# Optimization experiments

Hardware: AMD Instinct MI355X
Metric: run time of the kernel (lower is better)

Reference implementation:

```python
import jax, jax.numpy as jnp
import numpy as np

N_NODES = 50000
N_EDGES = 800000
HEADS = 4
OUT_CH = 64
NEG_SLOPE = 0.2  # PyG GATConv default


def gat_conv(x, edge_index, W, att_src, att_dst, bias):
    """PyG GATConv (concat=True, add_self_loops=True, eval mode).
    x: [N, F_in], edge_index: [2, E] (row 0 = src, row 1 = dst).
    W: [F_in, H*C], att_src/att_dst: [1, H, C], bias: [H*C].
    """
    n = x.shape[0]
    loops = jnp.arange(n, dtype=edge_index.dtype)
    src = jnp.concatenate([edge_index[0], loops])  # [E+N]
    dst = jnp.concatenate([edge_index[1], loops])

    h = (x @ W).reshape(n, HEADS, OUT_CH)           # [N, H, C]
    a_src = jnp.sum(h * att_src, axis=-1)           # [N, H]
    a_dst = jnp.sum(h * att_dst, axis=-1)           # [N, H]

    e = a_src[src] + a_dst[dst]                     # [E+N, H]
    e = jax.nn.leaky_relu(e, NEG_SLOPE)

    # segment softmax over incoming edges of each dst node
    e_max = jax.ops.segment_max(e, dst, num_segments=n)   # [N, H]
    e_exp = jnp.exp(e - e_max[dst])
    denom = jax.ops.segment_sum(e_exp, dst, num_segments=n)
    alpha = e_exp / (denom[dst] + 1e-16)            # [E+N, H]

    msg = h[src] * alpha[:, :, None]                # [E+N, H, C]
    out = jax.ops.segment_sum(msg, dst, num_segments=n)   # [N, H, C]
    return out.reshape(n, HEADS * OUT_CH) + bias


def setup_inputs() -> dict:
    key = jax.random.key(0)
    ks = jax.random.split(key, 10)
    d_in = 256
    d_hid = HEADS * OUT_CH  # 256
    s_in = 1.0 / np.sqrt(d_in)
    s_hid = 1.0 / np.sqrt(d_hid)
    return {
        "x": jax.random.normal(ks[0], (N_NODES, d_in), dtype=jnp.float32),
        "edge_index": jax.random.randint(ks[1], (2, N_EDGES), 0, N_NODES, dtype=jnp.int32),
        "W1": jax.random.normal(ks[2], (d_in, d_hid), dtype=jnp.float32) * s_in,
        "att_src1": jax.random.normal(ks[3], (1, HEADS, OUT_CH), dtype=jnp.float32) * s_hid,
        "att_dst1": jax.random.normal(ks[4], (1, HEADS, OUT_CH), dtype=jnp.float32) * s_hid,
        "b1": jnp.zeros((d_hid,), dtype=jnp.float32),
        "W2": jax.random.normal(ks[5], (d_hid, d_hid), dtype=jnp.float32) * s_hid,
        "att_src2": jax.random.normal(ks[6], (1, HEADS, OUT_CH), dtype=jnp.float32) * s_hid,
        "att_dst2": jax.random.normal(ks[7], (1, HEADS, OUT_CH), dtype=jnp.float32) * s_hid,
        "b2": jnp.zeros((d_hid,), dtype=jnp.float32),
    }


def reference(x, edge_index, W1, att_src1, att_dst1, b1, W2, att_src2, att_dst2, b2):
    # layer 1 + ELU (dropout is identity in eval mode)
    h = gat_conv(x, edge_index, W1, att_src1, att_dst1, b1)
    h = jax.nn.elu(h)
    # layer 2 + ELU
    h = gat_conv(h, edge_index, W2, att_src2, att_dst2, b2)
    h = jax.nn.elu(h)
    return h
```

## Files before the change

### kernel.cpp

```cpp
#include <hip/hip_runtime.h>
#include <hip/hip_bf16.h>

#define N_NODES 50000
#define N_EDGES 800000

typedef __attribute__((ext_vector_type(8))) short short8;
typedef __attribute__((ext_vector_type(4))) float floatx4;

__device__ __forceinline__ ushort f2bf(float f) {
    uint u = __float_as_uint(f);
    uint r = u + 0x7FFFu + ((u >> 16) & 1u);
    return (ushort)(r >> 16);
}
__device__ __forceinline__ float bfu2f(ushort h) {
    return __uint_as_float(((uint)h) << 16);
}
__device__ __forceinline__ float bflo(uint u) { return __uint_as_float(u << 16); }
__device__ __forceinline__ float bfhi(uint u) { return __uint_as_float(u & 0xffff0000u); }
__device__ __forceinline__ float lrelu(float e) { return e >= 0.f ? e : 0.2f * e; }

__global__ void deg_kernel(const int* __restrict__ dst, int* __restrict__ cnt, int E) {
    int i = blockIdx.x * blockDim.x + threadIdx.x;
    if (i < E) atomicAdd(&cnt[dst[i]], 1);
}

__global__ __launch_bounds__(256) void scan1_kernel(const int* __restrict__ cnt,
                                                    int* __restrict__ excl,
                                                    int* __restrict__ partial, int n) {
    __shared__ int sd[256];
    int tid = threadIdx.x;
    int i = blockIdx.x * 256 + tid;
    int v = (i < n) ? cnt[i] : 0;
    sd[tid] = v;
    __syncthreads();
    #pragma unroll
    for (int off = 1; off < 256; off <<= 1) {
        int t = (tid >= off) ? sd[tid - off] : 0;
        __syncthreads();
        sd[tid] += t;
        __syncthreads();
    }
    if (i < n) excl[i] = sd[tid] - v;
    if (tid == 255) partial[blockIdx.x] = sd[255];
}

__global__ __launch_bounds__(256) void scan2_kernel(int* __restrict__ partial, int nb) {
    __shared__ int sd[256];
    int tid = threadIdx.x;
    int v = (tid < nb) ? partial[tid] : 0;
    sd[tid] = v;
    __syncthreads();
    #pragma unroll
    for (int off = 1; off < 256; off <<= 1) {
        int t = (tid >= off) ? sd[tid - off] : 0;
        __syncthreads();
        sd[tid] += t;
        __syncthreads();
    }
    if (tid < nb) partial[tid] = sd[tid] - v;
}

__global__ __launch_bounds__(256) void scan3_kernel(const int* __restrict__ excl,
                                                    const int* __restrict__ partial,
                                                    int* __restrict__ row_ptr,
                                                    int* __restrict__ row_tmp, int n) {
    int i = blockIdx.x * 256 + threadIdx.x;
    if (i < n) {
        int v = excl[i] + partial[blockIdx.x];
        row_ptr[i] = v;
        row_tmp[i] = v;
    }
    if (i == 0) row_ptr[n] = N_EDGES;
}

__global__ void scatter_kernel(const int* __restrict__ src, const int* __restrict__ dst,
                               int* __restrict__ row_tmp, int* __restrict__ sorted_src,
                               int* __restrict__ sorted_dst, int E) {
    int i = blockIdx.x * blockDim.x + threadIdx.x;
    if (i < E) {
        int d = dst[i];
        int p = atomicAdd(&row_tmp[d], 1);
        sorted_src[p] = src[i];
        sorted_dst[p] = d;
    }
}

__global__ void prep_w(const float* __restrict__ W1, const float* __restrict__ W2,
                       ushort* __restrict__ Wt1_hi, ushort* __restrict__ Wt1_lo,
                       ushort* __restrict__ Wt2_hi, ushort* __restrict__ Wt2_lo) {
    int n = threadIdx.x, k = blockIdx.x & 255;
    const float* W = (blockIdx.x < 256) ? W1 : W2;
    ushort* Wh = (blockIdx.x < 256) ? Wt1_hi : Wt2_hi;
    ushort* Wl = (blockIdx.x < 256) ? Wt1_lo : Wt2_lo;
    float v = W[k * 256 + n];
    ushort hb = f2bf(v);
    Wh[n * 256 + k] = hb;
    Wl[n * 256 + k] = f2bf(v - bfu2f(hb));
}

__global__ __launch_bounds__(256) void gemm_att_kernel(const float* __restrict__ A,
                                                       const ushort* __restrict__ Wt_hi,
                                                       const ushort* __restrict__ Wt_lo,
                                                       const float* __restrict__ att_s,
                                                       const float* __restrict__ att_d,
                                                       ushort* __restrict__ H,
                                                       float* __restrict__ a_src,
                                                       float* __restrict__ a_dst, int M) {
    const int ROWP = 40;
    __shared__ ushort hi_s[128 * ROWP];
    __shared__ ushort lo_s[128 * ROWP];
    const int tid = threadIdx.x;
    const int wave = tid >> 6, lane = tid & 63;
    const int quad = lane >> 4, l16 = lane & 15;
    const int brow = blockIdx.x * 64;
    const int coff = blockIdx.y * 128;
    const int mrow = brow + wave * 16 + l16;
    const int mload = (mrow < M) ? mrow : (M - 1);

    floatx4 acc[8];
    #pragma unroll
    for (int t = 0; t < 8; t++) acc[t] = (floatx4){0.f, 0.f, 0.f, 0.f};

    for (int k0 = 0; k0 < 256; k0 += 32) {
        __syncthreads();
        {
            int t = tid & 127;
            const ushort* g = ((tid < 128) ? Wt_hi : Wt_lo) + (size_t)(coff + t) * 256 + k0;
            ushort* d = ((tid < 128) ? hi_s : lo_s) + t * ROWP;
            #pragma unroll
            for (int i = 0; i < 4; i++)
                *reinterpret_cast<short8*>(d + i * 8) =
                    *reinterpret_cast<const short8*>(g + i * 8);
        }
        __syncthreads();
        const float* ap = A + (size_t)mload * 256 + k0 + quad * 8;
        float4 a0 = *reinterpret_cast<const float4*>(ap);
        float4 a1 = *reinterpret_cast<const float4*>(ap + 4);
        float av[8] = {a0.x, a0.y, a0.z, a0.w, a1.x, a1.y, a1.z, a1.w};
        short8 a_hi, a_lo;
        #pragma unroll
        for (int j = 0; j < 8; j++) {
            ushort hb = f2bf(av[j]);
            a_hi[j] = (short)hb;
            a_lo[j] = (short)f2bf(av[j] - bfu2f(hb));
        }
        #pragma unroll
        for (int t = 0; t < 8; t++) {
            int roff = (t * 16 + l16) * ROWP + quad * 8;
            short8 b_hi = *reinterpret_cast<const short8*>(&hi_s[roff]);
            short8 b_lo = *reinterpret_cast<const short8*>(&lo_s[roff]);
            acc[t] = __builtin_amdgcn_mfma_f32_16x16x32_bf16(a_hi, b_hi, acc[t], 0, 0, 0);
            acc[t] = __builtin_amdgcn_mfma_f32_16x16x32_bf16(a_hi, b_lo, acc[t], 0, 0, 0);
            acc[t] = __builtin_amdgcn_mfma_f32_16x16x32_bf16(a_lo, b_hi, acc[t], 0, 0, 0);
        }
    }
    const int hb = blockIdx.y * 2;
    float ps[2][4] = {}, pd[2][4] = {};
    #pragma unroll
    for (int t = 0; t < 8; t++) {
        int hh = t >> 2;
        float as_v = att_s[coff + t * 16 + l16];
        float ad_v = att_d[coff + t * 16 + l16];
        #pragma unroll
        for (int r = 0; r < 4; r++) {
            ps[hh][r] += acc[t][r] * as_v;
            pd[hh][r] += acc[t][r] * ad_v;
        }
    }
    #pragma unroll
    for (int off = 1; off < 16; off <<= 1) {
        #pragma unroll
        for (int hh = 0; hh < 2; hh++)
            #pragma unroll
            for (int r = 0; r < 4; r++) {
                ps[hh][r] += __shfl_xor(ps[hh][r], off, 64);
                pd[hh][r] += __shfl_xor(pd[hh][r], off, 64);
            }
    }
    if (l16 == 0) {
        #pragma unroll
        for (int r = 0; r < 4; r++) {
            int m = brow + wave * 16 + quad * 4 + r;
            if (m < M) {
                #pragma unroll
                for (int hh = 0; hh < 2; hh++) {
                    a_src[m * 4 + hb + hh] = ps[hh][r];
                    a_dst[m * 4 + hb + hh] = pd[hh][r];
                }
            }
        }
    }
    #pragma unroll
    for (int t = 0; t < 8; t++) {
        int col = coff + t * 16 + l16;
        int c = col & 63, hh = col >> 6;
        #pragma unroll
        for (int r = 0; r < 4; r++) {
            int m = brow + wave * 16 + quad * 4 + r;
            if (m < M) H[(size_t)m * 256 + c * 4 + hh] = f2bf(acc[t][r]);
        }
    }
}

__global__ __launch_bounds__(256) void ew_kernel(const float* __restrict__ a_src,
                                                 const float* __restrict__ a_dst,
                                                 const int* __restrict__ sorted_src,
                                                 const int* __restrict__ sorted_dst,
                                                 float* __restrict__ ew, int E) {
    int j = blockIdx.x * 256 + threadIdx.x;
    if (j >= E) return;
    int s = sorted_src[j], d = sorted_dst[j];
    float4 as_ = *reinterpret_cast<const float4*>(a_src + (size_t)s * 4);
    float4 ad_ = *reinterpret_cast<const float4*>(a_dst + (size_t)d * 4);
    float4 w;
    w.x = __expf(lrelu(as_.x + ad_.x));
    w.y = __expf(lrelu(as_.y + ad_.y));
    w.z = __expf(lrelu(as_.z + ad_.z));
    w.w = __expf(lrelu(as_.w + ad_.w));
    *reinterpret_cast<float4*>(ew + (size_t)j * 4) = w;
}

__global__ __launch_bounds__(256) void agg_kernel(const ushort* __restrict__ H,
                                                  const float* __restrict__ a_src,
                                                  const float* __restrict__ a_dst,
                                                  const int* __restrict__ row_ptr,
                                                  const int* __restrict__ sorted_src,
                                                  const float* __restrict__ ew,
                                                  const float* __restrict__ bias,
                                                  float* __restrict__ out, int N) {
    int wave = threadIdx.x >> 6, lane = threadIdx.x & 63;
    int half = lane >> 5, hl = lane & 31;
    int i = blockIdx.x * 4 + wave;
    if (i >= N) return;
    float4 asv = *reinterpret_cast<const float4*>(a_src + (size_t)i * 4);
    float4 adv = *reinterpret_cast<const float4*>(a_dst + (size_t)i * 4);
    float ws0 = __expf(lrelu(asv.x + adv.x)), ws1 = __expf(lrelu(asv.y + adv.y));
    float ws2 = __expf(lrelu(asv.z + adv.z)), ws3 = __expf(lrelu(asv.w + adv.w));
    int start = row_ptr[i], end = row_ptr[i + 1];

    float a0 = 0.f, a1 = 0.f, a2 = 0.f, a3 = 0.f;
    float b0 = 0.f, b1 = 0.f, b2 = 0.f, b3 = 0.f;
    float dp0 = 0.f, dp1 = 0.f, dp2 = 0.f, dp3 = 0.f;

    for (int j = start + half; j < end; j += 2) {
        int sj = sorted_src[j];
        float4 w = *reinterpret_cast<const float4*>(ew + (size_t)j * 4);
        uint4 hv = *reinterpret_cast<const uint4*>(H + (size_t)sj * 256 + hl * 8);
        a0 += w.x * bflo(hv.x); a1 += w.y * bfhi(hv.x);
        a2 += w.z * bflo(hv.y); a3 += w.w * bfhi(hv.y);
        b0 += w.x * bflo(hv.z); b1 += w.y * bfhi(hv.z);
        b2 += w.z * bflo(hv.w); b3 += w.w * bfhi(hv.w);
        dp0 += w.x; dp1 += w.y; dp2 += w.z; dp3 += w.w;
    }
    a0 += __shfl_xor(a0, 32, 64); a1 += __shfl_xor(a1, 32, 64);
    a2 += __shfl_xor(a2, 32, 64); a3 += __shfl_xor(a3, 32, 64);
    b0 += __shfl_xor(b0, 32, 64); b1 += __shfl_xor(b1, 32, 64);
    b2 += __shfl_xor(b2, 32, 64); b3 += __shfl_xor(b3, 32, 64);
    dp0 += __shfl_xor(dp0, 32, 64); dp1 += __shfl_xor(dp1, 32, 64);
    dp2 += __shfl_xor(dp2, 32, 64); dp3 += __shfl_xor(dp3, 32, 64);
    {
        uint4 hv = *reinterpret_cast<const uint4*>(H + (size_t)i * 256 + hl * 8);
        a0 += ws0 * bflo(hv.x); a1 += ws1 * bfhi(hv.x);
        a2 += ws2 * bflo(hv.y); a3 += ws3 * bfhi(hv.y);
        b0 += ws0 * bflo(hv.z); b1 += ws1 * bfhi(hv.z);
        b2 += ws2 * bflo(hv.w); b3 += ws3 * bfhi(hv.w);
    }
    float r0 = 1.f / (dp0 + ws0 + 1e-16f), r1 = 1.f / (dp1 + ws1 + 1e-16f);
    float r2 = 1.f / (dp2 + ws2 + 1e-16f), r3 = 1.f / (dp3 + ws3 + 1e-16f);
    float* op = out + (size_t)i * 256 + hl * 2;
    float va = (half == 0) ? a0 : a2, vb = (half == 0) ? b0 : b2;
    float ra = (half == 0) ? r0 : r2;
    float va2 = (half == 0) ? a1 : a3, vb2 = (half == 0) ? b1 : b3;
    float ra2 = (half == 0) ? r1 : r3;
    int hofs = half * 128;
    float2 o;
    float v;
    v = va * ra + bias[hofs + 2 * hl];      o.x = (v > 0.f) ? v : expm1f(v);
    v = vb * ra + bias[hofs + 2 * hl + 1];  o.y = (v > 0.f) ? v : expm1f(v);
    *reinterpret_cast<float2*>(op + hofs) = o;
    v = va2 * ra2 + bias[hofs + 64 + 2 * hl];     o.x = (v > 0.f) ? v : expm1f(v);
    v = vb2 * ra2 + bias[hofs + 64 + 2 * hl + 1]; o.y = (v > 0.f) ? v : expm1f(v);
    *reinterpret_cast<float2*>(op + hofs + 64) = o;
}

extern "C" void kernel_launch(void* const* d_in, const int* in_sizes, int n_in,
                              void* d_out, int out_size, void* d_ws, size_t ws_size,
                              hipStream_t stream) {
    const float* x      = (const float*)d_in[0];
    const int*   eidx   = (const int*)d_in[1];
    const float* W1     = (const float*)d_in[2];
    const float* att_s1 = (const float*)d_in[3];
    const float* att_d1 = (const float*)d_in[4];
    const float* b1     = (const float*)d_in[5];
    const float* W2     = (const float*)d_in[6];
    const float* att_s2 = (const float*)d_in[7];
    const float* att_d2 = (const float*)d_in[8];
    const float* b2     = (const float*)d_in[9];
    float* out = (float*)d_out;

    const int N = N_NODES, E = N_EDGES;
    char* ws = (char*)d_ws;
    size_t off = 0;
    auto alloc = [&](size_t bytes) -> void* {
        void* p = ws + off;
        off += (bytes + 255) & ~(size_t)255;
        return p;
    };
    ushort* h       = (ushort*)alloc((size_t)N * 256 * sizeof(ushort));
    float*  ew      = (float*) alloc((size_t)E * 4 * sizeof(float));
    float*  a_src   = (float*) alloc((size_t)N * 4 * sizeof(float));
    float*  a_dst   = (float*) alloc((size_t)N * 4 * sizeof(float));
    int*    cnt     = (int*)   alloc((size_t)N * sizeof(int));
    int*    row_ptr = (int*)   alloc((size_t)(N + 1) * sizeof(int));
    int*    row_tmp = (int*)   alloc((size_t)N * sizeof(int));
    int*    sorted  = (int*)   alloc((size_t)E * sizeof(int));
    int*    sortedd = (int*)   alloc((size_t)E * sizeof(int));
    int*    excl    = (int*)   alloc((size_t)N * sizeof(int));
    int*    partial = (int*)   alloc(256 * sizeof(int));
    ushort* Wt1_hi  = (ushort*)alloc(256 * 256 * sizeof(ushort));
    ushort* Wt1_lo  = (ushort*)alloc(256 * 256 * sizeof(ushort));
    ushort* Wt2_hi  = (ushort*)alloc(256 * 256 * sizeof(ushort));
    ushort* Wt2_lo  = (ushort*)alloc(256 * 256 * sizeof(ushort));
    float*  x2      = out;
    (void)ws_size; (void)in_sizes; (void)n_in; (void)out_size;

    const int* e_src = eidx;
    const int* e_dst = eidx + E;
    const int nsb = (N + 255) / 256;
    const int neb = (E + 255) / 256;

    prep_w<<<512, 256, 0, stream>>>(W1, W2, Wt1_hi, Wt1_lo, Wt2_hi, Wt2_lo);
    hipMemsetAsync(cnt, 0, N * sizeof(int), stream);
    deg_kernel<<<neb, 256, 0, stream>>>(e_dst, cnt, E);
    scan1_kernel<<<nsb, 256, 0, stream>>>(cnt, excl, partial, N);
    scan2_kernel<<<1, 256, 0, stream>>>(partial, nsb);
    scan3_kernel<<<nsb, 256, 0, stream>>>(excl, partial, row_ptr, row_tmp, N);
    scatter_kernel<<<neb, 256, 0, stream>>>(e_src, e_dst, row_tmp, sorted, sortedd, E);

    dim3 ggrid((N + 63) / 64, 2);
    int nblk = (N + 3) / 4;
    gemm_att_kernel<<<ggrid, 256, 0, stream>>>(x, Wt1_hi, Wt1_lo, att_s1, att_d1,
                                               h, a_src, a_dst, N);
    ew_kernel<<<neb, 256, 0, stream>>>(a_src, a_dst, sorted, sortedd, ew, E);
    agg_kernel<<<nblk, 256, 0, stream>>>(h, a_src, a_dst, row_ptr, sorted, ew, b1, x2, N);
    gemm_att_kernel<<<ggrid, 256, 0, stream>>>(x2, Wt2_hi, Wt2_lo, att_s2, att_d2,
                                               h, a_src, a_dst, N);
    ew_kernel<<<neb, 256, 0, stream>>>(a_src, a_dst, sorted, sortedd, ew, E);
    agg_kernel<<<nblk, 256, 0, stream>>>(h, a_src, a_dst, row_ptr, sorted, ew, b2, out, N);
}
```

Measured before the change: 473.9 us.

## Restructure GAT aggregation: full wave per edge, batch eight edge gathers

Aggregation now assigns all 64 lanes of a wave to each edge, one channel and four heads per lane, instead of two half-waves each taking alternate edges. Eight edges are loaded per iteration (source ids, weights, 8-byte feature rows), so many gathers are in flight at once. This removes the cross-half shuffle reduction and halves the accumulator registers. The node index is made wave-uniform with readfirstlane, and outputs are written with nontemporal stores. The unguarded batch reads can run past the end of a node's edge list, and for the last node possibly past the edge arrays.

```diff
diff --git a/kernel.cpp b/kernel.cpp
--- a/kernel.cpp
+++ b/kernel.cpp
@@ -6,6 +6,7 @@
 
 typedef __attribute__((ext_vector_type(8))) short short8;
 typedef __attribute__((ext_vector_type(4))) float floatx4;
+typedef __attribute__((ext_vector_type(2))) uint uintx2;
 
 __device__ __forceinline__ ushort f2bf(float f) {
     uint u = __float_as_uint(f);
@@ -220,6 +221,13 @@
     *reinterpret_cast<float4*>(ew + (size_t)j * 4) = w;
 }
 
+#define AGG_ACC(W_, V_)                                                     \
+    do {                                                                    \
+        a0 += (W_).x * bflo((V_).x); a1 += (W_).y * bfhi((V_).x);           \
+        a2 += (W_).z * bflo((V_).y); a3 += (W_).w * bfhi((V_).y);           \
+        dp0 += (W_).x; dp1 += (W_).y; dp2 += (W_).z; dp3 += (W_).w;         \
+    } while (0)
+
 __global__ __launch_bounds__(256) void agg_kernel(const ushort* __restrict__ H,
                                                   const float* __restrict__ a_src,
                                                   const float* __restrict__ a_dst,
@@ -228,59 +236,57 @@
                                                   const float* __restrict__ ew,
                                                   const float* __restrict__ bias,
                                                   float* __restrict__ out, int N) {
-    int wave = threadIdx.x >> 6, lane = threadIdx.x & 63;
-    int half = lane >> 5, hl = lane & 31;
-    int i = blockIdx.x * 4 + wave;
+    const int lane = threadIdx.x & 63;
+    const int i = __builtin_amdgcn_readfirstlane(blockIdx.x * 4 + (threadIdx.x >> 6));
     if (i >= N) return;
-    float4 asv = *reinterpret_cast<const float4*>(a_src + (size_t)i * 4);
-    float4 adv = *reinterpret_cast<const float4*>(a_dst + (size_t)i * 4);
-    float ws0 = __expf(lrelu(asv.x + adv.x)), ws1 = __expf(lrelu(asv.y + adv.y));
-    float ws2 = __expf(lrelu(asv.z + adv.z)), ws3 = __expf(lrelu(asv.w + adv.w));
-    int start = row_ptr[i], end = row_ptr[i + 1];
+    const float4 asv = *reinterpret_cast<const float4*>(a_src + (size_t)i * 4);
+    const float4 adv = *reinterpret_cast<const float4*>(a_dst + (size_t)i * 4);
+    const float ws0 = __expf(lrelu(asv.x + adv.x)), ws1 = __expf(lrelu(asv.y + adv.y));
+    const float ws2 = __expf(lrelu(asv.z + adv.z)), ws3 = __expf(lrelu(asv.w + adv.w));
+    const int start = row_ptr[i], end = row_ptr[i + 1];
 
     float a0 = 0.f, a1 = 0.f, a2 = 0.f, a3 = 0.f;
-    float b0 = 0.f, b1 = 0.f, b2 = 0.f, b3 = 0.f;
     float dp0 = 0.f, dp1 = 0.f, dp2 = 0.f, dp3 = 0.f;
-
-    for (int j = start + half; j < end; j += 2) {
-        int sj = sorted_src[j];
-        float4 w = *reinterpret_cast<const float4*>(ew + (size_t)j * 4);
-        uint4 hv = *reinterpret_cast<const uint4*>(H + (size_t)sj * 256 + hl * 8);
-        a0 += w.x * bflo(hv.x); a1 += w.y * bfhi(hv.x);
-        a2 += w.z * bflo(hv.y); a3 += w.w * bfhi(hv.y);
-        b0 += w.x * bflo(hv.z); b1 += w.y * bfhi(hv.z);
-        b2 += w.z * bflo(hv.w); b3 += w.w * bfhi(hv.w);
-        dp0 += w.x; dp1 += w.y; dp2 += w.z; dp3 += w.w;
-    }
-    a0 += __shfl_xor(a0, 32, 64); a1 += __shfl_xor(a1, 32, 64);
-    a2 += __shfl_xor(a2, 32, 64); a3 += __shfl_xor(a3, 32, 64);
-    b0 += __shfl_xor(b0, 32, 64); b1 += __shfl_xor(b1, 32, 64);
-    b2 += __shfl_xor(b2, 32, 64); b3 += __shfl_xor(b3, 32, 64);
-    dp0 += __shfl_xor(dp0, 32, 64); dp1 += __shfl_xor(dp1, 32, 64);
-    dp2 += __shfl_xor(dp2, 32, 64); dp3 += __shfl_xor(dp3, 32, 64);
+    const ushort* __restrict__ Hl = H + lane * 4;
+
+    for (int j0 = start; j0 < end; j0 += 8) {
+        int s[8];
+        #pragma unroll
+        for (int k = 0; k < 8; k++) s[k] = sorted_src[j0 + k];
+        floatx4 w[8];
+        #pragma unroll
+        for (int k = 0; k < 8; k++)
+            w[k] = *reinterpret_cast<const floatx4*>(ew + (size_t)(j0 + k) * 4);
+        uintx2 hv[8];
+        #pragma unroll
+        for (int k = 0; k < 8; k++)
+            hv[k] = *reinterpret_cast<const uintx2*>(Hl + (size_t)s[k] * 256);
+        if (j0 + 8 <= end) {
+            #pragma unroll
+            for (int k = 0; k < 8; k++) AGG_ACC(w[k], hv[k]);
+        } else {
+            #pragma unroll
+            for (int k = 0; k < 8; k++)
+                if (j0 + k < end) AGG_ACC(w[k], hv[k]);
+        }
+    }
     {
-        uint4 hv = *reinterpret_cast<const uint4*>(H + (size_t)i * 256 + hl * 8);
+        uintx2 hv = *reinterpret_cast<const uintx2*>(Hl + (size_t)i * 256);
         a0 += ws0 * bflo(hv.x); a1 += ws1 * bfhi(hv.x);
         a2 += ws2 * bflo(hv.y); a3 += ws3 * bfhi(hv.y);
-        b0 += ws0 * bflo(hv.z); b1 += ws1 * bfhi(hv.z);
-        b2 += ws2 * bflo(hv.w); b3 += ws3 * bfhi(hv.w);
-    }
-    float r0 = 1.f / (dp0 + ws0 + 1e-16f), r1 = 1.f / (dp1 + ws1 + 1e-16f);
-    float r2 = 1.f / (dp2 + ws2 + 1e-16f), r3 = 1.f / (dp3 + ws3 + 1e-16f);
-    float* op = out + (size_t)i * 256 + hl * 2;
-    float va = (half == 0) ? a0 : a2, vb = (half == 0) ? b0 : b2;
-    float ra = (half == 0) ? r0 : r2;
-    float va2 = (half == 0) ? a1 : a3, vb2 = (half == 0) ? b1 : b3;
-    float ra2 = (half == 0) ? r1 : r3;
-    int hofs = half * 128;
-    float2 o;
+    }
+    const float r0 = 1.f / (dp0 + ws0 + 1e-16f), r1 = 1.f / (dp1 + ws1 + 1e-16f);
+    const float r2 = 1.f / (dp2 + ws2 + 1e-16f), r3 = 1.f / (dp3 + ws3 + 1e-16f);
+    float* op = out + (size_t)i * 256 + lane;
     float v;
-    v = va * ra + bias[hofs + 2 * hl];      o.x = (v > 0.f) ? v : expm1f(v);
-    v = vb * ra + bias[hofs + 2 * hl + 1];  o.y = (v > 0.f) ? v : expm1f(v);
-    *reinterpret_cast<float2*>(op + hofs) = o;
-    v = va2 * ra2 + bias[hofs + 64 + 2 * hl];     o.x = (v > 0.f) ? v : expm1f(v);
-    v = vb2 * ra2 + bias[hofs + 64 + 2 * hl + 1]; o.y = (v > 0.f) ? v : expm1f(v);
-    *reinterpret_cast<float2*>(op + hofs + 64) = o;
+    v = a0 * r0 + bias[lane];        v = (v > 0.f) ? v : expm1f(v);
+    __builtin_nontemporal_store(v, op);
+    v = a1 * r1 + bias[64 + lane];   v = (v > 0.f) ? v : expm1f(v);
+    __builtin_nontemporal_store(v, op + 64);
+    v = a2 * r2 + bias[128 + lane];  v = (v > 0.f) ? v : expm1f(v);
+    __builtin_nontemporal_store(v, op + 128);
+    v = a3 * r3 + bias[192 + lane];  v = (v > 0.f) ? v : expm1f(v);
+    __builtin_nontemporal_store(v, op + 192);
 }
 
 extern "C" void kernel_launch(void* const* d_in, const int* in_sizes, int n_in,
```

Result: faster. 461.0 us (-2.7%).
